# Optimization experiments

Hardware: AMD Instinct MI355X
Metric: run time of the kernel (lower is better)

## Reference

```python
import jax, jax.numpy as jnp
import numpy as np

N_NODES = 100000
N_EDGES = 1600000
N_GRAPHS = 256
IN_C = 64
C = 128
N_LAYERS = 5
LN_EPS = 1e-5


def setup_inputs() -> dict:
    key = jax.random.key(0)
    ks = jax.random.split(key, 16)
    x = jax.random.normal(ks[0], (N_NODES, IN_C), dtype=jnp.float32)
    edge_index = jax.random.randint(ks[1], (2, N_EDGES), 0, N_NODES, dtype=jnp.int32)
    batch = jnp.sort(jax.random.randint(ks[2], (N_NODES,), 0, N_GRAPHS, dtype=jnp.int32))
    s_in = 1.0 / np.sqrt(IN_C)
    s_c = 1.0 / np.sqrt(C)
    s_2c = 1.0 / np.sqrt(2 * C)
    return {
        "x": x,
        "edge_index": edge_index,
        "batch": batch,
        "proj_w": jax.random.uniform(ks[3], (IN_C, C), jnp.float32, -s_in, s_in),
        "proj_b": jax.random.uniform(ks[4], (C,), jnp.float32, -s_in, s_in),
        "gin_w1": jax.random.uniform(ks[5], (N_LAYERS, C, C), jnp.float32, -s_c, s_c),
        "gin_b1": jax.random.uniform(ks[6], (N_LAYERS, C), jnp.float32, -s_c, s_c),
        "gin_w2": jax.random.uniform(ks[7], (N_LAYERS, C, C), jnp.float32, -s_c, s_c),
        "gin_b2": jax.random.uniform(ks[8], (N_LAYERS, C), jnp.float32, -s_c, s_c),
        "ln_g": jnp.ones((N_LAYERS, C), jnp.float32),
        "ln_b": jnp.zeros((N_LAYERS, C), jnp.float32),
        "fw1": jax.random.uniform(ks[9], (C, 2 * C), jnp.float32, -s_c, s_c),
        "fb1": jax.random.uniform(ks[10], (2 * C,), jnp.float32, -s_c, s_c),
        "fw2": jax.random.uniform(ks[11], (2 * C, C), jnp.float32, -s_2c, s_2c),
        "fb2": jax.random.uniform(ks[12], (C,), jnp.float32, -s_2c, s_2c),
    }


def _layer_norm(h, g, b):
    mu = jnp.mean(h, axis=-1, keepdims=True)
    var = jnp.mean(jnp.square(h - mu), axis=-1, keepdims=True)
    return (h - mu) * jax.lax.rsqrt(var + LN_EPS) * g + b


def reference(x, edge_index, batch, proj_w, proj_b, gin_w1, gin_b1, gin_w2, gin_b2,
              ln_g, ln_b, fw1, fb1, fw2, fb2):
    src, dst = edge_index[0], edge_index[1]
    h = x @ proj_w + proj_b  # [N, C]
    for i in range(N_LAYERS):
        # GINConv (eps=0): mlp(x_i + sum_{j in N(i)} x_j)
        aggr = jax.ops.segment_sum(h[src], dst, num_segments=N_NODES)  # [N, C]
        z = h + aggr
        z = jax.nn.relu(z @ gin_w1[i] + gin_b1[i]) @ gin_w2[i] + gin_b2[i]
        h = _layer_norm(jax.nn.relu(z), ln_g[i], ln_b[i])
    # global add pool over graphs
    g = jax.ops.segment_sum(h, batch, num_segments=N_GRAPHS)  # [G, C]
    out = jax.nn.relu(g @ fw1 + fb1) @ fw2 + fb2  # [G, C]
    return out
```

## Files before the change

### kernel.cpp

```cpp
#include <hip/hip_runtime.h>
#include <hip/hip_bf16.h>

#define N_NODES  100000
#define N_EDGES  1600000
#define N_GRAPHS 256
#define CCH      128
#define INC      64
#define N_LAYERS 5
#define SLICE_N  12500
#define POOL_SPLIT 16
#define CAP      48

typedef __attribute__((ext_vector_type(8))) short  short8;
typedef __attribute__((ext_vector_type(4))) float  f32x4;

__device__ __forceinline__ float bits2f(unsigned int u){ union{unsigned int i; float f;} v; v.i=u; return v.f; }
__device__ __forceinline__ float b2f(unsigned short u){ return bits2f(((unsigned int)u)<<16); }
__device__ __forceinline__ float lo16(unsigned int u){ return bits2f(u<<16); }
__device__ __forceinline__ float hi16(unsigned int u){ return bits2f(u & 0xffff0000u); }
__device__ __forceinline__ unsigned short f2b(float f){
  union{float f; unsigned int i;} v; v.f=f;
  unsigned int r = v.i + 0x7fffu + ((v.i>>16)&1u);
  return (unsigned short)(r>>16);
}

__global__ __launch_bounds__(256) void cvt_kernel(const float* __restrict__ in,
                                                  unsigned short* __restrict__ out, int n){
  int i = (blockIdx.x*256 + threadIdx.x)*4;
  if (i >= n) return;
  float4 v = *(const float4*)(in + i);
  out[i+0] = f2b(v.x); out[i+1] = f2b(v.y); out[i+2] = f2b(v.z); out[i+3] = f2b(v.w);
}

__global__ void pack_kernel(const float* __restrict__ projw,
                            const float* __restrict__ w1,
                            const float* __restrict__ w2,
                            unsigned short* __restrict__ wp)
{
  int idx = blockIdx.x*256 + threadIdx.x;
  const float* src; int rem;
  if (idx < 8192) { src = projw; rem = idx; }
  else {
    int t2 = idx - 8192;
    int mat = t2 >> 14;
    rem = t2 & 16383;
    src = (mat < 5) ? (w1 + mat*16384) : (w2 + (mat-5)*16384);
  }
  int f    = rem >> 9;
  int lane = (rem >> 3) & 63;
  int j    = rem & 7;
  int kk = f >> 3, nn = f & 7;
  int k = kk*32 + (lane>>4)*8 + j;
  int n = nn*16 + (lane&15);
  wp[idx] = f2b(src[k*CCH + n]);
}

__global__ __launch_bounds__(256) void fill_kernel(const int* __restrict__ src, const int* __restrict__ dst,
                                                   int* __restrict__ cnt, int* __restrict__ esrc){
  int slice = blockIdx.x & 7;
  int lo = slice * SLICE_N, hi = lo + SLICE_N;
  int stride = (gridDim.x >> 3) * 256;
  for (int e = (blockIdx.x>>3)*256 + threadIdx.x; e < N_EDGES; e += stride){
    int d = dst[e];
    if (d >= lo && d < hi){
      int p = atomicAdd(&cnt[d], 1);
      if (p < CAP) esrc[(size_t)d*CAP + p] = src[e];
    }
  }
}

__global__ void bsearch_kernel(const int* __restrict__ batch, int* __restrict__ gstart){
  int g = threadIdx.x;
  int lo = 0, hi = N_NODES;
  while (lo < hi){
    int mid = (lo + hi) >> 1;
    if (batch[mid] < g) lo = mid + 1; else hi = mid;
  }
  gstart[g] = lo;
  if (g == 255) gstart[256] = N_NODES;
}

__global__ __launch_bounds__(256) void aggr_kernel(const unsigned short* __restrict__ h,
                                                   const int* __restrict__ cnt,
                                                   const int* __restrict__ esrc,
                                                   unsigned short* __restrict__ z)
{
  int node = blockIdx.x*4 + (threadIdx.x>>6);
  int lane = threadIdx.x & 63;
  int s = lane >> 4, c = lane & 15;
  const uint4* h16 = (const uint4*)h;
  float a[8];
  if (s == 0){
    uint4 v = h16[(size_t)node*16 + c];
    a[0]=lo16(v.x); a[1]=hi16(v.x); a[2]=lo16(v.y); a[3]=hi16(v.y);
    a[4]=lo16(v.z); a[5]=hi16(v.z); a[6]=lo16(v.w); a[7]=hi16(v.w);
  } else {
    #pragma unroll
    for (int k=0;k<8;k++) a[k] = 0.f;
  }
  int n = cnt[node]; if (n > CAP) n = CAP;
  const int* ep = esrc + (size_t)node*CAP;
  for (int e = s; e < n; e += 4){
    int sn = ep[e];
    uint4 r = h16[(size_t)sn*16 + c];
    a[0]+=lo16(r.x); a[1]+=hi16(r.x); a[2]+=lo16(r.y); a[3]+=hi16(r.y);
    a[4]+=lo16(r.z); a[5]+=hi16(r.z); a[6]+=lo16(r.w); a[7]+=hi16(r.w);
  }
  #pragma unroll
  for (int k=0;k<8;k++){
    a[k] += __shfl_xor(a[k], 16, 64);
    a[k] += __shfl_xor(a[k], 32, 64);
  }
  if (s == 0){
    uint4 o;
    o.x = (unsigned int)f2b(a[0]) | ((unsigned int)f2b(a[1])<<16);
    o.y = (unsigned int)f2b(a[2]) | ((unsigned int)f2b(a[3])<<16);
    o.z = (unsigned int)f2b(a[4]) | ((unsigned int)f2b(a[5])<<16);
    o.w = (unsigned int)f2b(a[6]) | ((unsigned int)f2b(a[7])<<16);
    ((uint4*)z)[(size_t)node*16 + c] = o;
  }
}

template<int KK, int MODE>
__global__ __launch_bounds__(256) void gemm_kernel(
    const unsigned short* __restrict__ A, int lda,
    const unsigned short* __restrict__ Wp,
    const float* __restrict__ bias,
    unsigned short* __restrict__ out,
    int M)
{
  const int tid = threadIdx.x;
  const int wave = tid>>6, lane = tid&63;
  const int rbase = blockIdx.x*128 + wave*32;
  if (rbase >= M) return;
  const int cl = lane & 15, rg = lane >> 4;
  const bool ok1 = (rbase + 16) < M;

  f32x4 acc[2][8];
  #pragma unroll
  for (int s=0;s<2;s++)
    #pragma unroll
    for (int nn=0;nn<8;nn++) acc[s][nn] = (f32x4){0.f,0.f,0.f,0.f};

  const short8* wp8 = (const short8*)Wp;
  #pragma unroll
  for (int kk=0;kk<KK;kk++){
    short8 bfr[8];
    #pragma unroll
    for (int nn=0;nn<8;nn++) bfr[nn] = wp8[(kk*8+nn)*64 + lane];
    const unsigned short* ap = A + (size_t)(rbase+cl)*lda + kk*32 + rg*8;
    short8 a0 = *(const short8*)ap;
    #pragma unroll
    for (int nn=0;nn<8;nn++)
      acc[0][nn] = __builtin_amdgcn_mfma_f32_16x16x32_bf16(a0, bfr[nn], acc[0][nn],0,0,0);
    if (ok1){
      short8 a1 = *(const short8*)(ap + (size_t)16*lda);
      #pragma unroll
      for (int nn=0;nn<8;nn++)
        acc[1][nn] = __builtin_amdgcn_mfma_f32_16x16x32_bf16(a1, bfr[nn], acc[1][nn],0,0,0);
    }
  }

  float bc[8];
  #pragma unroll
  for (int nn=0;nn<8;nn++) bc[nn] = bias[nn*16+cl];

  #pragma unroll
  for (int s=0;s<2;s++){
    if (s==1 && !ok1) break;
    const int rowb = rbase + s*16 + rg*4;
    #pragma unroll
    for (int j=0;j<4;j++){
      unsigned short* op = out + (size_t)(rowb+j)*CCH + cl;
      #pragma unroll
      for (int nn=0;nn<8;nn++){
        float t = acc[s][nn][j] + bc[nn];
        if (MODE>=1) t = fmaxf(t, 0.f);
        op[nn*16] = f2b(t);
      }
    }
  }
}

__global__ __launch_bounds__(256) void gemm12_kernel(
    const unsigned short* __restrict__ A,
    const unsigned short* __restrict__ Wp1,
    const float* __restrict__ b1,
    const unsigned short* __restrict__ Wp2,
    const float* __restrict__ b2,
    const float* __restrict__ lng,
    const float* __restrict__ lnb,
    unsigned short* __restrict__ out, int M)
{
  __shared__ unsigned short tl[4][32][136];
  const int tid = threadIdx.x;
  const int wave = tid>>6, lane = tid&63;
  const int rbase = blockIdx.x*128 + wave*32;
  if (rbase >= M) return;
  const int cl = lane & 15, rg = lane >> 4;
  const bool ok1 = (rbase + 16) < M;

  {
    f32x4 acc[2][8];
    #pragma unroll
    for (int s=0;s<2;s++)
      #pragma unroll
      for (int nn=0;nn<8;nn++) acc[s][nn] = (f32x4){0.f,0.f,0.f,0.f};

    const short8* wp8 = (const short8*)Wp1;
    #pragma unroll
    for (int kk=0;kk<4;kk++){
      short8 bfr[8];
      #pragma unroll
      for (int nn=0;nn<8;nn++) bfr[nn] = wp8[(kk*8+nn)*64 + lane];
      const unsigned short* ap = A + (size_t)(rbase+cl)*CCH + kk*32 + rg*8;
      short8 a0 = *(const short8*)ap;
      #pragma unroll
      for (int nn=0;nn<8;nn++)
        acc[0][nn] = __builtin_amdgcn_mfma_f32_16x16x32_bf16(a0, bfr[nn], acc[0][nn],0,0,0);
      if (ok1){
        short8 a1 = *(const short8*)(ap + (size_t)16*CCH);
        #pragma unroll
        for (int nn=0;nn<8;nn++)
          acc[1][nn] = __builtin_amdgcn_mfma_f32_16x16x32_bf16(a1, bfr[nn], acc[1][nn],0,0,0);
      }
    }
    float bc[8];
    #pragma unroll
    for (int nn=0;nn<8;nn++) bc[nn] = b1[nn*16+cl];
    #pragma unroll
    for (int s=0;s<2;s++){
      if (s==1 && !ok1) break;
      #pragma unroll
      for (int j=0;j<4;j++){
        int rel = s*16 + rg*4 + j;
        #pragma unroll
        for (int nn=0;nn<8;nn++){
          float t = acc[s][nn][j] + bc[nn];
          tl[wave][rel][nn*16+cl] = f2b(fmaxf(t, 0.f));
        }
      }
    }
  }
  {
    f32x4 acc[2][8];
    #pragma unroll
    for (int s=0;s<2;s++)
      #pragma unroll
      for (int nn=0;nn<8;nn++) acc[s][nn] = (f32x4){0.f,0.f,0.f,0.f};

    const short8* wp8 = (const short8*)Wp2;
    #pragma unroll
    for (int kk=0;kk<4;kk++){
      short8 bfr[8];
      #pragma unroll
      for (int nn=0;nn<8;nn++) bfr[nn] = wp8[(kk*8+nn)*64 + lane];
      short8 a0 = *(const short8*)&tl[wave][cl][kk*32 + rg*8];
      #pragma unroll
      for (int nn=0;nn<8;nn++)
        acc[0][nn] = __builtin_amdgcn_mfma_f32_16x16x32_bf16(a0, bfr[nn], acc[0][nn],0,0,0);
      if (ok1){
        short8 a1 = *(const short8*)&tl[wave][16+cl][kk*32 + rg*8];
        #pragma unroll
        for (int nn=0;nn<8;nn++)
          acc[1][nn] = __builtin_amdgcn_mfma_f32_16x16x32_bf16(a1, bfr[nn], acc[1][nn],0,0,0);
      }
    }
    float bc[8], gg[8], bb[8];
    #pragma unroll
    for (int nn=0;nn<8;nn++){
      bc[nn] = b2[nn*16+cl];
      gg[nn] = lng[nn*16+cl];
      bb[nn] = lnb[nn*16+cl];
    }
    #pragma unroll
    for (int s=0;s<2;s++){
      if (s==1 && !ok1) break;
      float v[8][4];
      #pragma unroll
      for (int nn=0;nn<8;nn++)
        #pragma unroll
        for (int j=0;j<4;j++)
          v[nn][j] = fmaxf(acc[s][nn][j] + bc[nn], 0.f);
      #pragma unroll
      for (int j=0;j<4;j++){
        float sm=0.f, sq=0.f;
        #pragma unroll
        for (int nn=0;nn<8;nn++){ sm += v[nn][j]; sq += v[nn][j]*v[nn][j]; }
        #pragma unroll
        for (int m=1;m<16;m<<=1){ sm += __shfl_xor(sm, m, 64); sq += __shfl_xor(sq, m, 64); }
        float mean = sm * (1.f/128.f);
        float var  = fmaxf(sq * (1.f/128.f) - mean*mean, 0.f);
        float rs = rsqrtf(var + 1e-5f);
        #pragma unroll
        for (int nn=0;nn<8;nn++) v[nn][j] = (v[nn][j]-mean)*rs*gg[nn] + bb[nn];
      }
      const int rowb = rbase + s*16 + rg*4;
      #pragma unroll
      for (int j=0;j<4;j++){
        unsigned short* op = out + (size_t)(rowb+j)*CCH + cl;
        #pragma unroll
        for (int nn=0;nn<8;nn++) op[nn*16] = f2b(v[nn][j]);
      }
    }
  }
}

__global__ __launch_bounds__(64) void pool1_kernel(const unsigned short* __restrict__ h,
                                                   const int* __restrict__ gstart,
                                                   float* __restrict__ gpart)
{
  int g = blockIdx.x >> 4;
  int sp = blockIdx.x & 15;
  int lane = threadIdx.x;
  int n0 = gstart[g], n1 = gstart[g+1];
  const unsigned int* hu = (const unsigned int*)h;
  float a0 = 0.f, a1 = 0.f;
  for (int n = n0 + sp; n < n1; n += POOL_SPLIT){
    unsigned int v = hu[(size_t)n*64 + lane];
    a0 += lo16(v); a1 += hi16(v);
  }
  float2* gp = (float2*)gpart;
  gp[(size_t)blockIdx.x*64 + lane] = make_float2(a0, a1);
}

__global__ __launch_bounds__(64) void pool2_kernel(const float* __restrict__ gpart,
                                                   float* __restrict__ gout)
{
  int g = blockIdx.x;
  int lane = threadIdx.x;
  const float2* gp = (const float2*)gpart;
  float a0 = 0.f, a1 = 0.f;
  #pragma unroll
  for (int sp=0; sp<POOL_SPLIT; sp++){
    float2 v = gp[((size_t)g*POOL_SPLIT + sp)*64 + lane];
    a0 += v.x; a1 += v.y;
  }
  ((float2*)gout)[(size_t)g*64 + lane] = make_float2(a0, a1);
}

__global__ __launch_bounds__(256) void final_kernel(const float* __restrict__ gout,
                                                    const float* __restrict__ fw1,
                                                    const float* __restrict__ fb1,
                                                    const float* __restrict__ fw2,
                                                    const float* __restrict__ fb2,
                                                    float* __restrict__ out)
{
  __shared__ float gr[128];
  __shared__ float hid[256];
  int g = blockIdx.x, t = threadIdx.x;
  if (t < 128) gr[t] = gout[g*CCH + t];
  __syncthreads();
  float a = 0.f;
  for (int k=0;k<128;k++) a += gr[k] * fw1[k*256 + t];
  a += fb1[t];
  hid[t] = fmaxf(a, 0.f);
  __syncthreads();
  if (t < 128){
    float o = 0.f;
    for (int j=0;j<256;j++) o += hid[j] * fw2[j*128 + t];
    o += fb2[t];
    out[(size_t)g*CCH + t] = o;
  }
}

extern "C" void kernel_launch(void* const* d_in, const int* in_sizes, int n_in,
                              void* d_out, int out_size, void* d_ws, size_t ws_size,
                              hipStream_t stream)
{
  const float* x     = (const float*)d_in[0];
  const int*   eidx  = (const int*)d_in[1];
  const int*   batch = (const int*)d_in[2];
  const float* projw = (const float*)d_in[3];
  const float* projb = (const float*)d_in[4];
  const float* gw1   = (const float*)d_in[5];
  const float* gb1   = (const float*)d_in[6];
  const float* gw2   = (const float*)d_in[7];
  const float* gb2   = (const float*)d_in[8];
  const float* lng   = (const float*)d_in[9];
  const float* lnb   = (const float*)d_in[10];
  const float* fw1   = (const float*)d_in[11];
  const float* fb1   = (const float*)d_in[12];
  const float* fw2   = (const float*)d_in[13];
  const float* fb2   = (const float*)d_in[14];

  const int* esrc_in = eidx;
  const int* edst_in = eidx + N_EDGES;

  char* w = (char*)d_ws; size_t off = 0;
  auto wsalloc = [&](size_t b)->char*{ char* p = w + off; off += (b + 255) & ~(size_t)255; return p; };
  unsigned short* Wp   = (unsigned short*)wsalloc(172032ull*2);
  unsigned short* xb   = (unsigned short*)wsalloc((size_t)N_NODES*INC*2);
  unsigned short* h    = (unsigned short*)wsalloc((size_t)N_NODES*CCH*2);
  unsigned short* z    = (unsigned short*)wsalloc((size_t)N_NODES*CCH*2);
  int*   cnt    = (int*)wsalloc((size_t)N_NODES*4);
  int*   esrc   = (int*)wsalloc((size_t)N_NODES*CAP*4);
  int*   gstart = (int*)wsalloc((N_GRAPHS+1)*4);
  float* gpart  = (float*)wsalloc((size_t)N_GRAPHS*POOL_SPLIT*CCH*4);
  float* gout   = (float*)wsalloc((size_t)N_GRAPHS*CCH*4);

  hipMemsetAsync(cnt, 0, (size_t)N_NODES*4, stream);

  cvt_kernel<<<6250, 256, 0, stream>>>(x, xb, N_NODES*INC);
  pack_kernel<<<672, 256, 0, stream>>>(projw, gw1, gw2, Wp);
  fill_kernel<<<2000, 256, 0, stream>>>(esrc_in, edst_in, cnt, esrc);
  bsearch_kernel<<<1, 256, 0, stream>>>(batch, gstart);

  gemm_kernel<2,0><<<782, 256, 0, stream>>>(xb, INC, Wp, projb, h, N_NODES);

  for (int L=0; L<N_LAYERS; ++L){
    aggr_kernel<<<25000, 256, 0, stream>>>(h, cnt, esrc, z);
    gemm12_kernel<<<782, 256, 0, stream>>>(z, Wp + 8192 + L*16384, gb1 + L*CCH,
                                           Wp + 8192 + (5+L)*16384, gb2 + L*CCH,
                                           lng + L*CCH, lnb + L*CCH, h, N_NODES);
  }

  pool1_kernel<<<N_GRAPHS*POOL_SPLIT, 64, 0, stream>>>(h, gstart, gpart);
  pool2_kernel<<<N_GRAPHS, 64, 0, stream>>>(gpart, gout);
  final_kernel<<<N_GRAPHS, 256, 0, stream>>>(gout, fw1, fb1, fw2, fb2, (float*)d_out);
}
```

Measured before the change: 595.6 us.

## Fuse neighbor aggregation into GIN MLP kernel and ping-pong node buffers

Removes the separate aggregation kernel. Each lane of the MLP kernel now gathers its row's neighbor features from the edge list, sums them in fp32 and packs the result directly into MFMA A-operands. This avoids writing and re-reading the intermediate z tensor every layer, and h is double-buffered so neighbor reads do not race with output writes. The trade-off is much less parallelism for the latency-bound gather: each lane walks a whole edge list serially, degrees differ within a wave, and register pressure rises. Separately, the edge-fill kernel uses nontemporal loads and reads src only for edges it keeps.

Result: slower. 676.9 us (+13.6%).

```diff
diff --git a/kernel.cpp b/kernel.cpp
--- a/kernel.cpp
+++ b/kernel.cpp
@@ -23,6 +23,8 @@
   unsigned int r = v.i + 0x7fffu + ((v.i>>16)&1u);
   return (unsigned short)(r>>16);
 }
+#define ACC8(a, r) { a[0]+=lo16(r.x); a[1]+=hi16(r.x); a[2]+=lo16(r.y); a[3]+=hi16(r.y); \
+                     a[4]+=lo16(r.z); a[5]+=hi16(r.z); a[6]+=lo16(r.w); a[7]+=hi16(r.w); }
 
 __global__ __launch_bounds__(256) void cvt_kernel(const float* __restrict__ in,
                                                   unsigned short* __restrict__ out, int n){
@@ -61,10 +63,11 @@
   int lo = slice * SLICE_N, hi = lo + SLICE_N;
   int stride = (gridDim.x >> 3) * 256;
   for (int e = (blockIdx.x>>3)*256 + threadIdx.x; e < N_EDGES; e += stride){
-    int d = dst[e];
+    int d = __builtin_nontemporal_load(&dst[e]);
     if (d >= lo && d < hi){
+      int s = __builtin_nontemporal_load(&src[e]);
       int p = atomicAdd(&cnt[d], 1);
-      if (p < CAP) esrc[(size_t)d*CAP + p] = src[e];
+      if (p < CAP) esrc[(size_t)d*CAP + p] = s;
     }
   }
 }
@@ -78,47 +81,6 @@
   }
   gstart[g] = lo;
   if (g == 255) gstart[256] = N_NODES;
-}
-
-__global__ __launch_bounds__(256) void aggr_kernel(const unsigned short* __restrict__ h,
-                                                   const int* __restrict__ cnt,
-                                                   const int* __restrict__ esrc,
-                                                   unsigned short* __restrict__ z)
-{
-  int node = blockIdx.x*4 + (threadIdx.x>>6);
-  int lane = threadIdx.x & 63;
-  int s = lane >> 4, c = lane & 15;
-  const uint4* h16 = (const uint4*)h;
-  float a[8];
-  if (s == 0){
-    uint4 v = h16[(size_t)node*16 + c];
-    a[0]=lo16(v.x); a[1]=hi16(v.x); a[2]=lo16(v.y); a[3]=hi16(v.y);
-    a[4]=lo16(v.z); a[5]=hi16(v.z); a[6]=lo16(v.w); a[7]=hi16(v.w);
-  } else {
-    #pragma unroll
-    for (int k=0;k<8;k++) a[k] = 0.f;
-  }
-  int n = cnt[node]; if (n > CAP) n = CAP;
-  const int* ep = esrc + (size_t)node*CAP;
-  for (int e = s; e < n; e += 4){
-    int sn = ep[e];
-    uint4 r = h16[(size_t)sn*16 + c];
-    a[0]+=lo16(r.x); a[1]+=hi16(r.x); a[2]+=lo16(r.y); a[3]+=hi16(r.y);
-    a[4]+=lo16(r.z); a[5]+=hi16(r.z); a[6]+=lo16(r.w); a[7]+=hi16(r.w);
-  }
-  #pragma unroll
-  for (int k=0;k<8;k++){
-    a[k] += __shfl_xor(a[k], 16, 64);
-    a[k] += __shfl_xor(a[k], 32, 64);
-  }
-  if (s == 0){
-    uint4 o;
-    o.x = (unsigned int)f2b(a[0]) | ((unsigned int)f2b(a[1])<<16);
-    o.y = (unsigned int)f2b(a[2]) | ((unsigned int)f2b(a[3])<<16);
-    o.z = (unsigned int)f2b(a[4]) | ((unsigned int)f2b(a[5])<<16);
-    o.w = (unsigned int)f2b(a[6]) | ((unsigned int)f2b(a[7])<<16);
-    ((uint4*)z)[(size_t)node*16 + c] = o;
-  }
 }
 
 template<int KK, int MODE>
@@ -183,7 +145,9 @@
 }
 
 __global__ __launch_bounds__(256) void gemm12_kernel(
-    const unsigned short* __restrict__ A,
+    const unsigned short* __restrict__ h,
+    const int* __restrict__ cnt,
+    const int* __restrict__ esrc,
     const unsigned short* __restrict__ Wp1,
     const float* __restrict__ b1,
     const unsigned short* __restrict__ Wp2,
@@ -199,6 +163,52 @@
   if (rbase >= M) return;
   const int cl = lane & 15, rg = lane >> 4;
   const bool ok1 = (rbase + 16) < M;
+  const uint4* h16 = (const uint4*)h;
+
+  short8 az[2][4];
+  #pragma unroll
+  for (int s=0;s<2;s++){
+    if (s==1 && !ok1) break;
+    int row = rbase + s*16 + cl;
+    float a[4][8];
+    const uint4* hr = h16 + (size_t)row*16;
+    #pragma unroll
+    for (int kk=0;kk<4;kk++){
+      uint4 v = hr[kk*4+rg];
+      a[kk][0]=lo16(v.x); a[kk][1]=hi16(v.x); a[kk][2]=lo16(v.y); a[kk][3]=hi16(v.y);
+      a[kk][4]=lo16(v.z); a[kk][5]=hi16(v.z); a[kk][6]=lo16(v.w); a[kk][7]=hi16(v.w);
+    }
+    int nb = cnt[row]; if (nb > CAP) nb = CAP;
+    const int* ep = esrc + (size_t)row*CAP;
+    int e = 0;
+    for (; e+2 <= nb; e += 2){
+      int s1 = ep[e], s2 = ep[e+1];
+      const uint4* h1 = h16 + (size_t)s1*16;
+      const uint4* h2 = h16 + (size_t)s2*16;
+      #pragma unroll
+      for (int kk=0;kk<4;kk++){
+        uint4 r1 = h1[kk*4+rg];
+        uint4 r2 = h2[kk*4+rg];
+        ACC8(a[kk], r1);
+        ACC8(a[kk], r2);
+      }
+    }
+    if (e < nb){
+      const uint4* h1 = h16 + (size_t)ep[e]*16;
+      #pragma unroll
+      for (int kk=0;kk<4;kk++){
+        uint4 r1 = h1[kk*4+rg];
+        ACC8(a[kk], r1);
+      }
+    }
+    #pragma unroll
+    for (int kk=0;kk<4;kk++){
+      short8 p;
+      #pragma unroll
+      for (int j=0;j<8;j++) p[j] = (short)f2b(a[kk][j]);
+      az[s][kk] = p;
+    }
+  }
 
   {
     f32x4 acc[2][8];
@@ -213,16 +223,13 @@
       short8 bfr[8];
       #pragma unroll
       for (int nn=0;nn<8;nn++) bfr[nn] = wp8[(kk*8+nn)*64 + lane];
-      const unsigned short* ap = A + (size_t)(rbase+cl)*CCH + kk*32 + rg*8;
-      short8 a0 = *(const short8*)ap;
       #pragma unroll
       for (int nn=0;nn<8;nn++)
-        acc[0][nn] = __builtin_amdgcn_mfma_f32_16x16x32_bf16(a0, bfr[nn], acc[0][nn],0,0,0);
+        acc[0][nn] = __builtin_amdgcn_mfma_f32_16x16x32_bf16(az[0][kk], bfr[nn], acc[0][nn],0,0,0);
       if (ok1){
-        short8 a1 = *(const short8*)(ap + (size_t)16*CCH);
         #pragma unroll
         for (int nn=0;nn<8;nn++)
-          acc[1][nn] = __builtin_amdgcn_mfma_f32_16x16x32_bf16(a1, bfr[nn], acc[1][nn],0,0,0);
+          acc[1][nn] = __builtin_amdgcn_mfma_f32_16x16x32_bf16(az[1][kk], bfr[nn], acc[1][nn],0,0,0);
       }
     }
     float bc[8];
@@ -392,7 +399,7 @@
   unsigned short* Wp   = (unsigned short*)wsalloc(172032ull*2);
   unsigned short* xb   = (unsigned short*)wsalloc((size_t)N_NODES*INC*2);
   unsigned short* h    = (unsigned short*)wsalloc((size_t)N_NODES*CCH*2);
-  unsigned short* z    = (unsigned short*)wsalloc((size_t)N_NODES*CCH*2);
+  unsigned short* h2   = (unsigned short*)wsalloc((size_t)N_NODES*CCH*2);
   int*   cnt    = (int*)wsalloc((size_t)N_NODES*4);
   int*   esrc   = (int*)wsalloc((size_t)N_NODES*CAP*4);
   int*   gstart = (int*)wsalloc((N_GRAPHS+1)*4);
@@ -408,14 +415,17 @@
 
   gemm_kernel<2,0><<<782, 256, 0, stream>>>(xb, INC, Wp, projb, h, N_NODES);
 
+  unsigned short* cur = h;
+  unsigned short* nxt = h2;
   for (int L=0; L<N_LAYERS; ++L){
-    aggr_kernel<<<25000, 256, 0, stream>>>(h, cnt, esrc, z);
-    gemm12_kernel<<<782, 256, 0, stream>>>(z, Wp + 8192 + L*16384, gb1 + L*CCH,
+    gemm12_kernel<<<782, 256, 0, stream>>>(cur, cnt, esrc,
+                                           Wp + 8192 + L*16384, gb1 + L*CCH,
                                            Wp + 8192 + (5+L)*16384, gb2 + L*CCH,
-                                           lng + L*CCH, lnb + L*CCH, h, N_NODES);
-  }
-
-  pool1_kernel<<<N_GRAPHS*POOL_SPLIT, 64, 0, stream>>>(h, gstart, gpart);
+                                           lng + L*CCH, lnb + L*CCH, nxt, N_NODES);
+    unsigned short* t = cur; cur = nxt; nxt = t;
+  }
+
+  pool1_kernel<<<N_GRAPHS*POOL_SPLIT, 64, 0, stream>>>(cur, gstart, gpart);
   pool2_kernel<<<N_GRAPHS, 64, 0, stream>>>(gpart, gout);
   final_kernel<<<N_GRAPHS, 256, 0, stream>>>(gout, fw1, fb1, fw2, fb2, (float*)d_out);
 }
```
